# Optimization experiments

Hardware: AMD Instinct MI355X
Metric: run time of the kernel (lower is better)

Reference implementation:

```python
import jax, jax.numpy as jnp
import numpy as np

B, S, H, DH, W, G, M = 2, 4096, 12, 64, 256, 64, 256
D = H * DH  # 768
VOCAB = 50282
NEG = -1e9


def setup_inputs() -> dict:
    key = jax.random.key(0)
    ks = jax.random.split(key, 16)
    f = lambda k, shp, s=0.02: jax.random.normal(k, shp, jnp.float32) * s
    return {
        'input_ids': jax.random.randint(ks[0], (B, S), 0, VOCAB, jnp.int32),
        'attn_mask': jnp.ones((B, S), jnp.float32),
        'html_idx': jnp.sort(jax.random.randint(ks[1], (B, M), 0, S, jnp.int32), axis=-1),
        'embed': f(ks[2], (VOCAB, D), 1.0),
        'Wq': f(ks[3], (D, D)), 'bq': jnp.zeros((D,), jnp.float32),
        'Wk': f(ks[4], (D, D)), 'bk': jnp.zeros((D,), jnp.float32),
        'Wv': f(ks[5], (D, D)), 'bv': jnp.zeros((D,), jnp.float32),
        'Wo': f(ks[6], (D, D)), 'bo': jnp.zeros((D,), jnp.float32),
        'gamma': jnp.ones((D,), jnp.float32), 'beta': jnp.zeros((D,), jnp.float32),
        'Wp': f(ks[7], (D, D)), 'bp': jnp.zeros((D,), jnp.float32),
        'Wa': f(ks[8], (D, 3)), 'ba': jnp.zeros((3,), jnp.float32),
        'Ws': f(ks[9], (D, 2)), 'bs': jnp.zeros((2,), jnp.float32),
    }


def _band_shift(t, n_chunks):
    # t: [..., n_chunks+2, W, ...chunked along axis -3/-2]; gather 3 neighbor chunks
    return jnp.concatenate([t[..., i:i + n_chunks, :, :] for i in range(3)], axis=-2)


def longformer_hpt(input_ids, attn_mask, html_idx, embed, Wq, bq, Wk, bk, Wv, bv,
                   Wo, bo, gamma, beta, Wp, bp, Wa, ba, Ws, bs):
    x = embed[input_ids]  # [B,S,D]
    heads = lambda t: t.reshape(B, S, H, DH).transpose(0, 2, 1, 3)  # [B,H,S,DH]
    q, k, v = heads(x @ Wq + bq), heads(x @ Wk + bk), heads(x @ Wv + bv)
    scale = 1.0 / np.sqrt(DH).astype(np.float32)
    C = S // W  # chunks

    # --- sliding-window (banded) attention, one-sided window W ---
    kp = jnp.pad(k, ((0, 0), (0, 0), (W, W), (0, 0))).reshape(B, H, C + 2, W, DH)
    vp = jnp.pad(v, ((0, 0), (0, 0), (W, W), (0, 0))).reshape(B, H, C + 2, W, DH)
    k3 = _band_shift(kp, C)  # [B,H,C,3W,DH]
    v3 = _band_shift(vp, C)
    qc = q.reshape(B, H, C, W, DH)
    sb = jnp.einsum('bhcqd,bhckd->bhcqk', qc, k3) * scale  # [B,H,C,W,3W]

    ii = jnp.arange(W)[:, None]
    jj = jnp.arange(3 * W)[None, :]
    band_ok = jnp.abs(jj - W - ii) <= W  # [W,3W]
    keypos = jnp.arange(C)[:, None] * W - W + jnp.arange(3 * W)[None, :]  # [C,3W]
    kvalid = (keypos >= 0) & (keypos < S) & (keypos >= G)  # global keys handled separately
    mp = jnp.pad(attn_mask, ((0, 0), (W, W))).reshape(B, C + 2, W)
    m3 = jnp.concatenate([mp[:, i:i + C] for i in range(3)], axis=2)  # [B,C,3W]
    mask = band_ok[None, :, :] & kvalid[:, None, :] & (m3[:, :, None, :] > 0)[..., :, :].reshape(B, C, 1, 3 * W).astype(bool) if False else (band_ok[None, None, :, :] & kvalid[None, :, None, :] & (m3[:, :, None, :] > 0))  # [B,C,W,3W]
    sb = jnp.where(mask[:, None], sb, NEG).reshape(B, H, S, 3 * W)

    # --- all tokens also attend to the G global tokens ---
    kg, vg = k[:, :, :G], v[:, :, :G]
    sg = jnp.einsum('bhsd,bhgd->bhsg', q, kg) * scale
    sg = jnp.where(attn_mask[:, None, None, :G] > 0, sg, NEG)

    p = jax.nn.softmax(jnp.concatenate([sg, sb], -1), -1)  # [B,H,S,G+3W]
    pg, pb = p[..., :G], p[..., G:].reshape(B, H, C, W, 3 * W)
    out = (jnp.einsum('bhcqk,bhckd->bhcqd', pb, v3).reshape(B, H, S, DH)
           + jnp.einsum('bhsg,bhgd->bhsd', pg, vg))

    # --- global queries attend to everything ---
    sgl = jnp.einsum('bhgd,bhsd->bhgs', q[:, :, :G], k) * scale
    sgl = jnp.where(attn_mask[:, None, None, :] > 0, sgl, NEG)
    outg = jnp.einsum('bhgs,bhsd->bhgd', jax.nn.softmax(sgl, -1), v)
    out = jnp.concatenate([outg, out[:, :, G:]], axis=2)

    ctx = out.transpose(0, 2, 1, 3).reshape(B, S, D)
    h = x + ctx @ Wo + bo
    mu = h.mean(-1, keepdims=True)
    var = ((h - mu) ** 2).mean(-1, keepdims=True)
    hn = (h - mu) / jnp.sqrt(var + 1e-5) * gamma + beta  # last_hidden [B,S,D]

    # probes (ans_probe: Linear(768,3)+Sigmoid, span_probe: Linear(768,2)+Sigmoid)
    ans = jax.nn.sigmoid(hn @ Wa + ba)
    span = jax.nn.sigmoid(hn @ Ws + bs)

    # ReIndexer gather of HTML-element hidden states + ConditionCalculator
    hr = jnp.take_along_axis(hn, html_idx[:, :, None].astype(jnp.int32), axis=1)  # [B,M,D]
    t = jax.nn.relu(hr @ Wp + bp)
    cond = jax.nn.sigmoid(jnp.einsum('bqh,bch->bcq', hr, t))  # [B,M,M]
    return hn, ans, span, cond


def reference(input_ids, attn_mask, html_idx, embed, Wq, bq, Wk, bk, Wv, bv,
              Wo, bo, gamma, beta, Wp, bp, Wa, ba, Ws, bs):
    return longformer_hpt(input_ids, attn_mask, html_idx, embed, Wq, bq, Wk, bk,
                          Wv, bv, Wo, bo, gamma, beta, Wp, bp, Wa, ba, Ws, bs)
```

## Files before the change

### kernel.cpp

```cpp
#include <hip/hip_runtime.h>

typedef unsigned short u16;
typedef unsigned int   u32;
typedef __attribute__((ext_vector_type(8))) short s8v;
typedef __attribute__((ext_vector_type(8))) unsigned short us8;
typedef __attribute__((ext_vector_type(4))) float f4v;

constexpr int BC  = 2;
constexpr int SL  = 4096;
constexpr int NH  = 12;
constexpr int HD  = 64;
constexpr int DM  = 768;
constexpr int WIN = 256;
constexpr int GLB = 64;
constexpr int QN  = 2304;
constexpr int KCH = 32;
constexpr float FOLD = 0.125f * 1.44269504088896f;
constexpr float NEGS = -1.0e9f;
constexpr float DEFER = 44.36f;

__device__ __forceinline__ float b2f(u16 b){ return __uint_as_float(((u32)b) << 16); }
__device__ __forceinline__ u16 f2b(float f){
  u32 u = __float_as_uint(f);
  return (u16)((u + 0x7fffu + ((u >> 16) & 1u)) >> 16);
}
__device__ __forceinline__ float wredsum(float v){
  #pragma unroll
  for (int o = 32; o > 0; o >>= 1) v += __shfl_xor(v, o, 64);
  return v;
}
__device__ __forceinline__ float sigf(float x){ return 1.f / (1.f + __expf(-x)); }

__global__ void pack_embed(const float* __restrict__ Wq, const float* __restrict__ Wk,
                           const float* __restrict__ Wv, const float* __restrict__ Wo,
                           const float* __restrict__ Wp,
                           const float* __restrict__ bq, const float* __restrict__ bk,
                           const float* __restrict__ bv,
                           u16* __restrict__ wt_qkv, u16* __restrict__ wt_o,
                           u16* __restrict__ wt_p, float* __restrict__ b_qkv,
                           const int* __restrict__ ids, const float* __restrict__ emb,
                           u16* __restrict__ xb)
{
  __shared__ float tile[64][65];
  const int bid = blockIdx.x;
  const int t = threadIdx.x;
  if (bid < 720){
    const int mi = bid / 144, rest = bid % 144;
    const int kt = rest / 12, ntc = rest % 12;
    const float* src = (mi==0)?Wq:(mi==1)?Wk:(mi==2)?Wv:(mi==3)?Wo:Wp;
    u16* dst = (mi<3) ? (wt_qkv + (size_t)mi*768*768) : ((mi==3) ? wt_o : wt_p);
    const int k0 = kt*64, n0 = ntc*64;
    #pragma unroll
    for (int i=0;i<4;i++){
      const int r = (t>>4) + i*16;
      float4 v = ((const float4*)(src + (long)(k0+r)*768 + n0))[t&15];
      tile[r][(t&15)*4+0] = v.x; tile[r][(t&15)*4+1] = v.y;
      tile[r][(t&15)*4+2] = v.z; tile[r][(t&15)*4+3] = v.w;
    }
    __syncthreads();
    const int n = t & 63, kc = (t>>6)*16;
    u32* d32 = (u32*)(dst + (long)(n0+n)*768 + k0 + kc);
    #pragma unroll
    for (int i=0;i<8;i++){
      d32[i] = (u32)f2b(tile[kc+2*i][n]) | ((u32)f2b(tile[kc+2*i+1][n]) << 16);
    }
    if (bid < 9){
      const int i = bid*256 + t;
      if (i < 2304) b_qkv[i] = (i < 768) ? bq[i] : (i < 1536) ? bk[i-768] : bv[i-1536];
    }
  } else {
    int e4 = (bid-720)*256 + t;
    int row = e4 / 192, d4 = e4 - row*192;
    int id = ids[row];
    float4 v = ((const float4*)(emb + (long)id*768))[d4];
    u32 p0 = (u32)f2b(v.x) | ((u32)f2b(v.y) << 16);
    u32 p1 = (u32)f2b(v.z) | ((u32)f2b(v.w) << 16);
    ((u32*)(xb + (long)row*768))[d4*2]   = p0;
    ((u32*)(xb + (long)row*768))[d4*2+1] = p1;
  }
}

__global__ void gather_hr(const int* __restrict__ hidx, const float* __restrict__ hn,
                          u16* __restrict__ hrb){
  int e = blockIdx.x*256 + threadIdx.x;
  if (e >= 512*768) return;
  int r = e / 768, d = e - r*768;
  int b = r >> 8;
  int idx = hidx[r];
  hrb[e] = f2b(hn[((long)(b*SL + idx))*768 + d]);
}

template<int MODE, bool SWZ>
__global__ __launch_bounds__(256, 2)
void gemm_bt(const u16* __restrict__ A, const u16* __restrict__ Bt,
             const float* __restrict__ bias, const u16* __restrict__ resB,
             float* __restrict__ outF, u16* __restrict__ outB,
             int M, int N, int K, long sA, long sB, long sO)
{
  const int bz = blockIdx.z;
  A  += (long)bz * sA;
  Bt += (long)bz * sB;
  int vid = blockIdx.x + gridDim.x*blockIdx.y;
  if constexpr (SWZ){
    const int chunk = (gridDim.x*gridDim.y) >> 3;
    vid = (vid & 7)*chunk + (vid >> 3);
  }
  const int n0 = (vid % gridDim.x) * 128;
  const int m0 = (vid / gridDim.x) * 128;
  __shared__ u16 lsA[128*64];
  __shared__ u16 lsB[128*64];
  const int t = threadIdx.x;
  const int w = t >> 6, lane = t & 63;
  const int wr = w >> 1, wc = w & 1;
  const int fr = lane & 15, fq = lane >> 4;

  f4v acc[4][4];
  #pragma unroll
  for (int i=0;i<4;i++)
    #pragma unroll
    for (int j=0;j<4;j++) acc[i][j] = (f4v)0.f;

  for (int k0 = 0; k0 < K; k0 += 64){
    #pragma unroll
    for (int i=0;i<4;i++){
      int e = (w*4+i)*512 + lane*8;
      int row = e >> 6, col = e & 63;
      __builtin_amdgcn_global_load_lds(
        (const __attribute__((address_space(1))) void*)(A + (long)(m0+row)*K + (k0+col)),
        (__attribute__((address_space(3))) void*)(&lsA[(w*4+i)*512]), 16, 0, 0);
      __builtin_amdgcn_global_load_lds(
        (const __attribute__((address_space(1))) void*)(Bt + (long)(n0+row)*K + (k0+col)),
        (__attribute__((address_space(3))) void*)(&lsB[(w*4+i)*512]), 16, 0, 0);
    }
    __syncthreads();
    #pragma unroll
    for (int kk = 0; kk < 2; kk++){
      s8v af[4], bfv[4];
      #pragma unroll
      for (int mi=0;mi<4;mi++)
        af[mi] = *(const s8v*)&lsA[(wr*64 + mi*16 + fr)*64 + kk*32 + fq*8];
      #pragma unroll
      for (int ni=0;ni<4;ni++)
        bfv[ni] = *(const s8v*)&lsB[(wc*64 + ni*16 + fr)*64 + kk*32 + fq*8];
      #pragma unroll
      for (int mi=0;mi<4;mi++)
        #pragma unroll
        for (int ni=0;ni<4;ni++)
          acc[mi][ni] = __builtin_amdgcn_mfma_f32_16x16x32_bf16(af[mi], bfv[ni], acc[mi][ni], 0, 0, 0);
    }
    __syncthreads();
  }
  #pragma unroll
  for (int mi=0;mi<4;mi++){
    #pragma unroll
    for (int ni=0;ni<4;ni++){
      #pragma unroll
      for (int r=0;r<4;r++){
        int row = m0 + wr*64 + mi*16 + fq*4 + r;
        int col = n0 + wc*64 + ni*16 + fr;
        float v = acc[mi][ni][r];
        if constexpr (MODE == 0){
          v += bias[col];
          outB[(long)row*N + col] = f2b(v);
        } else if constexpr (MODE == 1){
          v += bias[col] + b2f(resB[(long)row*N + col]);
          outB[(long)row*N + col] = f2b(v);
        } else if constexpr (MODE == 2){
          v = fmaxf(v + bias[col], 0.f);
          outB[(long)row*N + col] = f2b(v);
        } else {
          (outF + bz*sO)[(long)row*N + col] = sigf(v);
        }
      }
    }
  }
}

__global__ __launch_bounds__(256, 4)
void attn_band_mfma(const u16* __restrict__ qkv, const float* __restrict__ mask, u16* __restrict__ ctx)
{
  const int q0 = blockIdx.x * 64;
  const int h = blockIdx.y, b = blockIdx.z;
  const int t = threadIdx.x;
  const int w = t >> 6, lane = t & 63;
  const int fq = lane >> 4, fr = lane & 15;

  __shared__ u16 lsK[64*64];
  __shared__ u16 lsVT[2][64*72];
  __shared__ u16 lsP[4][16*72];
  __shared__ float lsM[2][64];

  const long bq = (long)b*SL*QN;
  const u16* qrow = qkv + (bq + (long)(q0 + w*16 + fr)*QN) + h*HD;
  s8v aq[2];
  aq[0] = *(const s8v*)(qrow + fq*8);
  aq[1] = *(const s8v*)(qrow + 32 + fq*8);

  s8v ones_bf;
  {
    const short o = (fr == 0) ? (short)0x3F80 : (short)0;
    #pragma unroll
    for (int j=0;j<8;j++) ones_bf[j] = o;
  }

  const u16* kq = qkv + bq + DM + h*HD;
  const u16* vq = qkv + bq + 2*DM + h*HD;
  const float* mrow = mask + b*SL;

  const int ti_lo = (q0 < 320) ? ((320 - q0) >> 6) : 0;
  const int ti_hi_raw = (4352 - q0) >> 6;
  const int ti_hi = ti_hi_raw < 9 ? ti_hi_raw : 9;
  const int NTT = 1 + (ti_hi - ti_lo);
  const int kb0 = q0 - 256 + ti_lo*64;

  f4v out[4];
  f4v outl = (f4v)0.f;
  #pragma unroll
  for (int n=0;n<4;n++) out[n] = (f4v)0.f;
  float m = -3.0e38f;

  us8 vv0, vv1;
  auto stage_issue = [&](int i, int vbuf){
    const int k0 = (i == 0) ? 0 : kb0 + (i-1)*64;
    if (t < 64) lsM[vbuf][t] = mrow[k0 + t];
    #pragma unroll
    for (int j=0;j<2;j++){
      const int r = (w*2+j)*8 + (lane>>3);
      const int d = ((lane&7) ^ (lane>>3))*8;
      __builtin_amdgcn_global_load_lds(
        (const __attribute__((address_space(1))) void*)(kq + (long)(k0+r)*QN + d),
        (__attribute__((address_space(3))) void*)(&lsK[(w*2+j)*512]), 16, 0, 0);
    }
    vv0 = *(const us8*)(vq + (long)(k0+lane)*QN + w*8);
    vv1 = *(const us8*)(vq + (long)(k0+lane)*QN + w*8 + 32);
  };

  stage_issue(0, 0);
  int cur = 0;
  for (int i = 0; i < NTT; i++){
    const int k0 = (i == 0) ? 0 : kb0 + (i-1)*64;
    const int d0 = w*8;
    #pragma unroll
    for (int jj=0;jj<8;jj++) lsVT[cur][(d0+jj)*72 + lane] = (u16)vv0[jj];
    #pragma unroll
    for (int jj=0;jj<8;jj++) lsVT[cur][(d0+32+jj)*72 + lane] = (u16)vv1[jj];
    __syncthreads();

    f4v s[4];
    #pragma unroll
    for (int n=0;n<4;n++) s[n] = (f4v)0.f;
    #pragma unroll
    for (int kk=0;kk<2;kk++){
      #pragma unroll
      for (int n=0;n<4;n++){
        s8v bf = *(const s8v*)&lsK[(16*n+fr)*64 + (((kk*4+fq) ^ (fr&7))<<3)];
        s[n] = __builtin_amdgcn_mfma_f32_16x16x32_bf16(aq[kk], bf, s[n], 0,0,0);
      }
    }
    __syncthreads();
    if (i+1 < NTT) stage_issue(i+1, cur^1);

    const bool isg = (i == 0);
    const int dlt = k0 - q0 - w*16;
    const bool maskAll = __all(lsM[cur][lane] > 0.f);
    const bool fullOK = maskAll && (isg || (dlt >= -241 && dlt <= 193));
    if (!fullOK){
      #pragma unroll
      for (int n=0;n<4;n++){
        const int kcol = 16*n + fr;
        const float mk = lsM[cur][kcol];
        #pragma unroll
        for (int r=0;r<4;r++){
          const int dd = k0 + kcol - (q0 + w*16 + fq*4 + r);
          const bool valid = (mk > 0.f) && (isg || (dd >= -WIN && dd <= WIN));
          s[n][r] = valid ? s[n][r] : NEGS;
        }
      }
    }
    float rmloc = fmaxf(fmaxf(fmaxf(s[0][0],s[0][1]),fmaxf(s[0][2],s[0][3])),
                        fmaxf(fmaxf(s[1][0],s[1][1]),fmaxf(s[1][2],s[1][3])));
    rmloc = fmaxf(rmloc, fmaxf(fmaxf(fmaxf(s[2][0],s[2][1]),fmaxf(s[2][2],s[2][3])),
                               fmaxf(fmaxf(s[3][0],s[3][1]),fmaxf(s[3][2],s[3][3]))));
    if (__any(rmloc > m + DEFER)){
      float rm = rmloc;
      rm = fmaxf(rm, __shfl_xor(rm, 1, 64));
      rm = fmaxf(rm, __shfl_xor(rm, 2, 64));
      rm = fmaxf(rm, __shfl_xor(rm, 4, 64));
      rm = fmaxf(rm, __shfl_xor(rm, 8, 64));
      const float mn = fmaxf(m, rm);
      const float sf = exp2f((m - mn)*FOLD);
      m = mn;
      outl *= sf;
      #pragma unroll
      for (int n=0;n<4;n++)
        #pragma unroll
        for (int r=0;r<4;r++) out[n][r] *= sf;
    }
    const float mF = m * FOLD;
    u16* lsPw = lsP[w];
    #pragma unroll
    for (int r=0;r<4;r++){
      const float p0 = exp2f(fmaf(s[0][r], FOLD, -mF));
      const float p1 = exp2f(fmaf(s[1][r], FOLD, -mF));
      const float p2 = exp2f(fmaf(s[2][r], FOLD, -mF));
      const float p3 = exp2f(fmaf(s[3][r], FOLD, -mF));
      u32 a, c;
      asm("v_cvt_pk_bf16_f32 %0, %1, %2" : "=v"(a) : "v"(p0), "v"(p1));
      asm("v_cvt_pk_bf16_f32 %0, %1, %2" : "=v"(c) : "v"(p2), "v"(p3));
      const int row = (fq*4+r)*72;
      lsPw[row + fr]      = (u16)a;
      lsPw[row + 16 + fr] = (u16)(a >> 16);
      lsPw[row + 32 + fr] = (u16)c;
      lsPw[row + 48 + fr] = (u16)(c >> 16);
    }
    s8v ap[2];
    ap[0] = *(const s8v*)&lsPw[fr*72 + fq*8];
    ap[1] = *(const s8v*)&lsPw[fr*72 + 32 + fq*8];
    #pragma unroll
    for (int kk=0;kk<2;kk++){
      #pragma unroll
      for (int n=0;n<4;n++){
        s8v bv = *(const s8v*)&lsVT[cur][(16*n+fr)*72 + kk*32 + fq*8];
        out[n] = __builtin_amdgcn_mfma_f32_16x16x32_bf16(ap[kk], bv, out[n], 0,0,0);
      }
      outl = __builtin_amdgcn_mfma_f32_16x16x32_bf16(ap[kk], ones_bf, outl, 0,0,0);
    }
    cur ^= 1;
  }
  float linv[4];
  #pragma unroll
  for (int r=0;r<4;r++) linv[r] = 1.f / __shfl(outl[r], lane & 48, 64);
  u16* cb = ctx + (((long)(b*SL) + q0 + w*16 + fq*4))*DM + h*HD + fr;
  #pragma unroll
  for (int n=0;n<4;n++)
    #pragma unroll
    for (int r=0;r<4;r++)
      cb[(long)r*DM + 16*n] = f2b(out[n][r]*linv[r]);
}

__global__ __launch_bounds__(256, 4)
void attn_global_part(const u16* __restrict__ qkv, const float* __restrict__ mask,
                      float* __restrict__ pout, float* __restrict__ pml)
{
  const int ck = blockIdx.x;
  const int h = blockIdx.y, b = blockIdx.z;
  const int bh = b*NH + h;
  const int t = threadIdx.x;
  const int w = t >> 6, lane = t & 63;
  const int fq = lane >> 4, fr = lane & 15;

  __shared__ u16 lsK[64*64];
  __shared__ u16 lsVT[2][64*72];
  __shared__ u16 lsP[4][16*72];
  __shared__ float lsM[2][64];

  const long bq = (long)b*SL*QN;
  const u16* qrow = qkv + (bq + (long)(w*16 + fr)*QN) + h*HD;
  s8v aq[2];
  aq[0] = *(const s8v*)(qrow + fq*8);
  aq[1] = *(const s8v*)(qrow + 32 + fq*8);

  s8v ones_bf;
  {
    const short o = (fr == 0) ? (short)0x3F80 : (short)0;
    #pragma unroll
    for (int j=0;j<8;j++) ones_bf[j] = o;
  }

  const u16* kq = qkv + bq + DM + h*HD;
  const u16* vq = qkv + bq + 2*DM + h*HD;
  const float* mrow = mask + b*SL;

  f4v out[4];
  f4v outl = (f4v)0.f;
  #pragma unroll
  for (int n=0;n<4;n++) out[n] = (f4v)0.f;
  float m = -3.0e38f;

  us8 vv0, vv1;
  auto stage_issue = [&](int i, int vbuf){
    const int k0 = ck*128 + i*64;
    if (t < 64) lsM[vbuf][t] = mrow[k0 + t];
    #pragma unroll
    for (int j=0;j<2;j++){
      const int r = (w*2+j)*8 + (lane>>3);
      const int d = ((lane&7) ^ (lane>>3))*8;
      __builtin_amdgcn_global_load_lds(
        (const __attribute__((address_space(1))) void*)(kq + (long)(k0+r)*QN + d),
        (__attribute__((address_space(3))) void*)(&lsK[(w*2+j)*512]), 16, 0, 0);
    }
    vv0 = *(const us8*)(vq + (long)(k0+lane)*QN + w*8);
    vv1 = *(const us8*)(vq + (long)(k0+lane)*QN + w*8 + 32);
  };

  stage_issue(0, 0);
  int cur = 0;
  for (int i = 0; i < 2; i++){
    const int d0 = w*8;
    #pragma unroll
    for (int jj=0;jj<8;jj++) lsVT[cur][(d0+jj)*72 + lane] = (u16)vv0[jj];
    #pragma unroll
    for (int jj=0;jj<8;jj++) lsVT[cur][(d0+32+jj)*72 + lane] = (u16)vv1[jj];
    __syncthreads();

    f4v s[4];
    #pragma unroll
    for (int n=0;n<4;n++) s[n] = (f4v)0.f;
    #pragma unroll
    for (int kk=0;kk<2;kk++){
      #pragma unroll
      for (int n=0;n<4;n++){
        s8v bf = *(const s8v*)&lsK[(16*n+fr)*64 + (((kk*4+fq) ^ (fr&7))<<3)];
        s[n] = __builtin_amdgcn_mfma_f32_16x16x32_bf16(aq[kk], bf, s[n], 0,0,0);
      }
    }
    __syncthreads();
    if (i+1 < 2) stage_issue(i+1, cur^1);

    const bool fullOK = __all(lsM[cur][lane] > 0.f);
    if (!fullOK){
      #pragma unroll
      for (int n=0;n<4;n++){
        const float mk = lsM[cur][16*n + fr];
        #pragma unroll
        for (int r=0;r<4;r++)
          s[n][r] = (mk > 0.f) ? s[n][r] : NEGS;
      }
    }
    float rmloc = fmaxf(fmaxf(fmaxf(s[0][0],s[0][1]),fmaxf(s[0][2],s[0][3])),
                        fmaxf(fmaxf(s[1][0],s[1][1]),fmaxf(s[1][2],s[1][3])));
    rmloc = fmaxf(rmloc, fmaxf(fmaxf(fmaxf(s[2][0],s[2][1]),fmaxf(s[2][2],s[2][3])),
                               fmaxf(fmaxf(s[3][0],s[3][1]),fmaxf(s[3][2],s[3][3]))));
    if (__any(rmloc > m + DEFER)){
      float rm = rmloc;
      rm = fmaxf(rm, __shfl_xor(rm, 1, 64));
      rm = fmaxf(rm, __shfl_xor(rm, 2, 64));
      rm = fmaxf(rm, __shfl_xor(rm, 4, 64));
      rm = fmaxf(rm, __shfl_xor(rm, 8, 64));
      const float mn = fmaxf(m, rm);
      const float sf = exp2f((m - mn)*FOLD);
      m = mn;
      outl *= sf;
      #pragma unroll
      for (int n=0;n<4;n++)
        #pragma unroll
        for (int r=0;r<4;r++) out[n][r] *= sf;
    }
    const float mF = m * FOLD;
    u16* lsPw = lsP[w];
    #pragma unroll
    for (int r=0;r<4;r++){
      const float p0 = exp2f(fmaf(s[0][r], FOLD, -mF));
      const float p1 = exp2f(fmaf(s[1][r], FOLD, -mF));
      const float p2 = exp2f(fmaf(s[2][r], FOLD, -mF));
      const float p3 = exp2f(fmaf(s[3][r], FOLD, -mF));
      u32 a, c;
      asm("v_cvt_pk_bf16_f32 %0, %1, %2" : "=v"(a) : "v"(p0), "v"(p1));
      asm("v_cvt_pk_bf16_f32 %0, %1, %2" : "=v"(c) : "v"(p2), "v"(p3));
      const int row = (fq*4+r)*72;
      lsPw[row + fr]      = (u16)a;
      lsPw[row + 16 + fr] = (u16)(a >> 16);
      lsPw[row + 32 + fr] = (u16)c;
      lsPw[row + 48 + fr] = (u16)(c >> 16);
    }
    s8v ap[2];
    ap[0] = *(const s8v*)&lsPw[fr*72 + fq*8];
    ap[1] = *(const s8v*)&lsPw[fr*72 + 32 + fq*8];
    #pragma unroll
    for (int kk=0;kk<2;kk++){
      #pragma unroll
      for (int n=0;n<4;n++){
        s8v bv = *(const s8v*)&lsVT[cur][(16*n+fr)*72 + kk*32 + fq*8];
        out[n] = __builtin_amdgcn_mfma_f32_16x16x32_bf16(ap[kk], bv, out[n], 0,0,0);
      }
      outl = __builtin_amdgcn_mfma_f32_16x16x32_bf16(ap[kk], ones_bf, outl, 0,0,0);
    }
    cur ^= 1;
  }
  float* pob = pout + ((long)(ck*BC*NH + bh))*64*64;
  #pragma unroll
  for (int n=0;n<4;n++)
    #pragma unroll
    for (int r=0;r<4;r++)
      pob[(w*16 + fq*4 + r)*64 + 16*n + fr] = out[n][r];
  if (fr == 0){
    float* pmb = pml + ((long)(ck*BC*NH + bh))*128;
    #pragma unroll
    for (int r=0;r<4;r++){
      pmb[(w*16 + fq*4 + r)*2 + 0] = m * FOLD;
      pmb[(w*16 + fq*4 + r)*2 + 1] = outl[r];
    }
  }
}

__global__ __launch_bounds__(256, 2)
void attn_global_combine(const float* __restrict__ pout, const float* __restrict__ pml,
                         u16* __restrict__ ctx)
{
  const int bh = blockIdx.x;
  const int b = bh / NH, h = bh % NH;
  const int t = threadIdx.x;
  __shared__ float wgt[KCH][64];
  __shared__ float rl[64];
  if (t < 64){
    float mc[KCH], lc[KCH];
    #pragma unroll
    for (int c = 0; c < KCH; c++){
      const float* pmb = pml + ((long)(c*BC*NH + bh))*128 + t*2;
      mc[c] = pmb[0]; lc[c] = pmb[1];
    }
    float M = mc[0];
    #pragma unroll
    for (int c = 1; c < KCH; c++) M = fmaxf(M, mc[c]);
    float L = 0.f;
    #pragma unroll
    for (int c = 0; c < KCH; c++){
      const float wv = exp2f(mc[c] - M);
      wgt[c][t] = wv;
      L += lc[c]*wv;
    }
    rl[t] = 1.f/L;
  }
  __syncthreads();
  const int row = t >> 2, dseg = t & 3;
  float acc[16];
  #pragma unroll
  for (int i=0;i<16;i++) acc[i] = 0.f;
  for (int c = 0; c < KCH; c++){
    const float wv = wgt[c][row];
    const float4* pb = (const float4*)(pout + ((long)(c*BC*NH + bh)*64 + row)*64 + dseg*16);
    #pragma unroll
    for (int i = 0; i < 4; i++){
      float4 v = pb[i];
      acc[i*4+0] += v.x*wv; acc[i*4+1] += v.y*wv;
      acc[i*4+2] += v.z*wv; acc[i*4+3] += v.w*wv;
    }
  }
  u16* cr = ctx + ((long)(b*SL + row))*DM + h*HD + dseg*16;
  const float r = rl[row];
  #pragma unroll
  for (int i = 0; i < 16; i += 2){
    u32 pk = (u32)f2b(acc[i]*r) | ((u32)f2b(acc[i+1]*r) << 16);
    *(u32*)(cr + i) = pk;
  }
}

__global__ __launch_bounds__(384, 2)
void ln_heads(const u16* __restrict__ hb, const float* __restrict__ gamma, const float* __restrict__ beta,
              const float* __restrict__ Wa, const float* __restrict__ ba,
              const float* __restrict__ Wsp, const float* __restrict__ bsp,
              float* __restrict__ hn, float* __restrict__ ans, float* __restrict__ span)
{
  const int r = blockIdx.x;
  const int t = threadIdx.x, lane = t & 63, w = t >> 6;
  __shared__ float red[12];
  __shared__ float dred[6][5];
  const u32 pk = ((const u32*)(hb + (long)r*DM))[t];
  const float v0 = b2f((u16)(pk & 0xffff));
  const float v1 = b2f((u16)(pk >> 16));
  float sum = wredsum(v0 + v1);
  float sq  = wredsum(v0*v0 + v1*v1);
  if (lane == 0){ red[w] = sum; red[6+w] = sq; }
  __syncthreads();
  float mu = 0.f, msq = 0.f;
  #pragma unroll
  for (int i=0;i<6;i++){ mu += red[i]; msq += red[6+i]; }
  mu *= (1.f/768.f); msq *= (1.f/768.f);
  const float rstd = rsqrtf(msq - mu*mu + 1e-5f);
  const int i0 = 2*t, i1 = 2*t+1;
  const float y0 = (v0 - mu)*rstd*gamma[i0] + beta[i0];
  const float y1 = (v1 - mu)*rstd*gamma[i1] + beta[i1];
  ((float2*)(hn + (long)r*DM))[t] = make_float2(y0, y1);
  float pa0 = y0*Wa[i0*3+0] + y1*Wa[i1*3+0];
  float pa1 = y0*Wa[i0*3+1] + y1*Wa[i1*3+1];
  float pa2 = y0*Wa[i0*3+2] + y1*Wa[i1*3+2];
  float ps0 = y0*Wsp[i0*2+0] + y1*Wsp[i1*2+0];
  float ps1 = y0*Wsp[i0*2+1] + y1*Wsp[i1*2+1];
  pa0 = wredsum(pa0); pa1 = wredsum(pa1); pa2 = wredsum(pa2);
  ps0 = wredsum(ps0); ps1 = wredsum(ps1);
  if (lane == 0){ dred[w][0]=pa0; dred[w][1]=pa1; dred[w][2]=pa2; dred[w][3]=ps0; dred[w][4]=ps1; }
  __syncthreads();
  if (t == 0){
    float A0=0,A1=0,A2=0,S0=0,S1=0;
    #pragma unroll
    for (int i=0;i<6;i++){ A0+=dred[i][0]; A1+=dred[i][1]; A2+=dred[i][2]; S0+=dred[i][3]; S1+=dred[i][4]; }
    ans[(long)r*3+0]  = sigf(A0 + ba[0]);
    ans[(long)r*3+1]  = sigf(A1 + ba[1]);
    ans[(long)r*3+2]  = sigf(A2 + ba[2]);
    span[(long)r*2+0] = sigf(S0 + bsp[0]);
    span[(long)r*2+1] = sigf(S1 + bsp[1]);
  }
}

extern "C" void kernel_launch(void* const* d_in, const int* in_sizes, int n_in,
                              void* d_out, int out_size, void* d_ws, size_t ws_size,
                              hipStream_t stream)
{
  const int*   input_ids = (const int*)  d_in[0];
  const float* attn_mask = (const float*)d_in[1];
  const int*   html_idx  = (const int*)  d_in[2];
  const float* embed     = (const float*)d_in[3];
  const float* Wq = (const float*)d_in[4];  const float* bq = (const float*)d_in[5];
  const float* Wk = (const float*)d_in[6];  const float* bk = (const float*)d_in[7];
  const float* Wv = (const float*)d_in[8];  const float* bv = (const float*)d_in[9];
  const float* Wo = (const float*)d_in[10]; const float* bo = (const float*)d_in[11];
  const float* gamma = (const float*)d_in[12]; const float* beta = (const float*)d_in[13];
  const float* Wp = (const float*)d_in[14]; const float* bp = (const float*)d_in[15];
  const float* Wa = (const float*)d_in[16]; const float* ba = (const float*)d_in[17];
  const float* Wsp = (const float*)d_in[18]; const float* bsp = (const float*)d_in[19];

  char* ws = (char*)d_ws;
  size_t off = 0;
  auto take = [&](size_t bytes)->char*{
    char* p = ws + off; off += (bytes + 255) & ~(size_t)255; return p;
  };
  u16*   x_b    = (u16*)  take((size_t)8192*768*2);
  u16*   wt_qkv = (u16*)  take((size_t)2304*768*2);
  u16*   wt_o   = (u16*)  take((size_t)768*768*2);
  u16*   wt_p   = (u16*)  take((size_t)768*768*2);
  float* b_qkv  = (float*)take(2304*4);
  u16*   qkv_b  = (u16*)  take((size_t)8192*2304*2);
  u16*   ctx_b  = (u16*)  take((size_t)8192*768*2);
  u16*   h_b    = (u16*)  take((size_t)8192*768*2);
  u16*   hr_b   = (u16*)  take((size_t)512*768*2);
  u16*   t_b    = (u16*)  take((size_t)512*768*2);
  float* pout   = (float*)take((size_t)KCH*BC*NH*64*64*4);
  float* pml    = (float*)take((size_t)KCH*BC*NH*128*4);

  float* out_hn   = (float*)d_out;
  float* out_ans  = out_hn  + (size_t)8192*768;
  float* out_span = out_ans + (size_t)8192*3;
  float* out_cond = out_span + (size_t)8192*2;

  pack_embed<<<6864, 256, 0, stream>>>(Wq, Wk, Wv, Wo, Wp, bq, bk, bv,
                                       wt_qkv, wt_o, wt_p, b_qkv,
                                       input_ids, embed, x_b);

  gemm_bt<0,true><<<dim3(18,64,1), 256, 0, stream>>>(x_b, wt_qkv, b_qkv, nullptr,
                                                nullptr, qkv_b, 8192, 2304, 768, 0,0,0);
  attn_band_mfma<<<dim3(64,12,2), 256, 0, stream>>>(qkv_b, attn_mask, ctx_b);
  attn_global_part<<<dim3(KCH,12,2), 256, 0, stream>>>(qkv_b, attn_mask, pout, pml);
  attn_global_combine<<<BC*NH, 256, 0, stream>>>(pout, pml, ctx_b);
  gemm_bt<1,true><<<dim3(6,64,1), 256, 0, stream>>>(ctx_b, wt_o, bo, x_b,
                                               nullptr, h_b, 8192, 768, 768, 0,0,0);
  ln_heads<<<8192, 384, 0, stream>>>(h_b, gamma, beta, Wa, ba, Wsp, bsp,
                                     out_hn, out_ans, out_span);
  gather_hr<<<1536, 256, 0, stream>>>(html_idx, out_hn, hr_b);
  gemm_bt<2,false><<<dim3(6,4,1), 256, 0, stream>>>(hr_b, wt_p, bp, nullptr,
                                              nullptr, t_b, 512, 768, 768, 0,0,0);
  gemm_bt<3,false><<<dim3(2,2,2), 256, 0, stream>>>(t_b, hr_b, nullptr, nullptr,
                                              out_cond, nullptr, 256, 256, 768,
                                              (long)256*768, (long)256*768, (long)256*256);
}
```

Baseline: 221.9 us.

## Pack V transpose into 32-bit LDS stores and skip global-query block

The V tile transpose into shared memory now has each lane load 4-element slices from two adjacent key rows and write packed pairs as 32-bit stores, replacing sixteen 16-bit scattered stores per lane. This halves LDS store instructions and should reduce bank conflicts during the transpose. Separately, the band attention grid drops the first 64-query block, presumably because the global-attention kernels already overwrite those rows. That relies on the combine kernel fully producing the first 64 query rows of ctx.

```diff
diff --git a/kernel.cpp b/kernel.cpp
--- a/kernel.cpp
+++ b/kernel.cpp
@@ -4,6 +4,7 @@
 typedef unsigned int   u32;
 typedef __attribute__((ext_vector_type(8))) short s8v;
 typedef __attribute__((ext_vector_type(8))) unsigned short us8;
+typedef __attribute__((ext_vector_type(4))) unsigned short us4;
 typedef __attribute__((ext_vector_type(4))) float f4v;
 
 constexpr int BC  = 2;
@@ -179,7 +180,7 @@
 __global__ __launch_bounds__(256, 4)
 void attn_band_mfma(const u16* __restrict__ qkv, const float* __restrict__ mask, u16* __restrict__ ctx)
 {
-  const int q0 = blockIdx.x * 64;
+  const int q0 = (blockIdx.x + 1) * 64;
   const int h = blockIdx.y, b = blockIdx.z;
   const int t = threadIdx.x;
   const int w = t >> 6, lane = t & 63;
@@ -219,7 +220,10 @@
   for (int n=0;n<4;n++) out[n] = (f4v)0.f;
   float m = -3.0e38f;
 
-  us8 vv0, vv1;
+  const int k2 = lane & 31, dq = lane >> 5;
+  const int dd0 = w*8 + dq*4;
+
+  us4 va0, vb0, va1, vb1;
   auto stage_issue = [&](int i, int vbuf){
     const int k0 = (i == 0) ? 0 : kb0 + (i-1)*64;
     if (t < 64) lsM[vbuf][t] = mrow[k0 + t];
@@ -231,19 +235,25 @@
         (const __attribute__((address_space(1))) void*)(kq + (long)(k0+r)*QN + d),
         (__attribute__((address_space(3))) void*)(&lsK[(w*2+j)*512]), 16, 0, 0);
     }
-    vv0 = *(const us8*)(vq + (long)(k0+lane)*QN + w*8);
-    vv1 = *(const us8*)(vq + (long)(k0+lane)*QN + w*8 + 32);
+    const u16* v0 = vq + (long)(k0+2*k2)*QN;
+    const u16* v1 = vq + (long)(k0+2*k2+1)*QN;
+    va0 = *(const us4*)(v0 + dd0);
+    vb0 = *(const us4*)(v1 + dd0);
+    va1 = *(const us4*)(v0 + dd0 + 32);
+    vb1 = *(const us4*)(v1 + dd0 + 32);
   };
 
   stage_issue(0, 0);
   int cur = 0;
   for (int i = 0; i < NTT; i++){
     const int k0 = (i == 0) ? 0 : kb0 + (i-1)*64;
-    const int d0 = w*8;
-    #pragma unroll
-    for (int jj=0;jj<8;jj++) lsVT[cur][(d0+jj)*72 + lane] = (u16)vv0[jj];
-    #pragma unroll
-    for (int jj=0;jj<8;jj++) lsVT[cur][(d0+32+jj)*72 + lane] = (u16)vv1[jj];
+    #pragma unroll
+    for (int j=0;j<4;j++){
+      const u32 pk0 = (u32)va0[j] | ((u32)vb0[j] << 16);
+      *(u32*)&lsVT[cur][(dd0+j)*72 + 2*k2] = pk0;
+      const u32 pk1 = (u32)va1[j] | ((u32)vb1[j] << 16);
+      *(u32*)&lsVT[cur][(dd0+32+j)*72 + 2*k2] = pk1;
+    }
     __syncthreads();
 
     f4v s[4];
@@ -377,7 +387,10 @@
   for (int n=0;n<4;n++) out[n] = (f4v)0.f;
   float m = -3.0e38f;
 
-  us8 vv0, vv1;
+  const int k2 = lane & 31, dq = lane >> 5;
+  const int dd0 = w*8 + dq*4;
+
+  us4 va0, vb0, va1, vb1;
   auto stage_issue = [&](int i, int vbuf){
     const int k0 = ck*128 + i*64;
     if (t < 64) lsM[vbuf][t] = mrow[k0 + t];
@@ -389,18 +402,24 @@
         (const __attribute__((address_space(1))) void*)(kq + (long)(k0+r)*QN + d),
         (__attribute__((address_space(3))) void*)(&lsK[(w*2+j)*512]), 16, 0, 0);
     }
-    vv0 = *(const us8*)(vq + (long)(k0+lane)*QN + w*8);
-    vv1 = *(const us8*)(vq + (long)(k0+lane)*QN + w*8 + 32);
+    const u16* v0 = vq + (long)(k0+2*k2)*QN;
+    const u16* v1 = vq + (long)(k0+2*k2+1)*QN;
+    va0 = *(const us4*)(v0 + dd0);
+    vb0 = *(const us4*)(v1 + dd0);
+    va1 = *(const us4*)(v0 + dd0 + 32);
+    vb1 = *(const us4*)(v1 + dd0 + 32);
   };
 
   stage_issue(0, 0);
   int cur = 0;
   for (int i = 0; i < 2; i++){
-    const int d0 = w*8;
-    #pragma unroll
-    for (int jj=0;jj<8;jj++) lsVT[cur][(d0+jj)*72 + lane] = (u16)vv0[jj];
-    #pragma unroll
-    for (int jj=0;jj<8;jj++) lsVT[cur][(d0+32+jj)*72 + lane] = (u16)vv1[jj];
+    #pragma unroll
+    for (int j=0;j<4;j++){
+      const u32 pk0 = (u32)va0[j] | ((u32)vb0[j] << 16);
+      *(u32*)&lsVT[cur][(dd0+j)*72 + 2*k2] = pk0;
+      const u32 pk1 = (u32)va1[j] | ((u32)vb1[j] << 16);
+      *(u32*)&lsVT[cur][(dd0+32+j)*72 + 2*k2] = pk1;
+    }
     __syncthreads();
 
     f4v s[4];
@@ -638,7 +657,7 @@
 
   gemm_bt<0,true><<<dim3(18,64,1), 256, 0, stream>>>(x_b, wt_qkv, b_qkv, nullptr,
                                                 nullptr, qkv_b, 8192, 2304, 768, 0,0,0);
-  attn_band_mfma<<<dim3(64,12,2), 256, 0, stream>>>(qkv_b, attn_mask, ctx_b);
+  attn_band_mfma<<<dim3(63,12,2), 256, 0, stream>>>(qkv_b, attn_mask, ctx_b);
   attn_global_part<<<dim3(KCH,12,2), 256, 0, stream>>>(qkv_b, attn_mask, pout, pml);
   attn_global_combine<<<BC*NH, 256, 0, stream>>>(pout, pml, ctx_b);
   gemm_bt<1,true><<<dim3(6,64,1), 256, 0, stream>>>(ctx_b, wt_o, bo, x_b,
```

Result: no change. 226.3 us (+2.0%).
